# Kernel optimization log

Hardware: AMD Instinct MI355X
Metric: run time of the kernel (lower is better)

Reference implementation:

```python
import jax, jax.numpy as jnp
import numpy as np

B, T, S, O, D = 1024, 512, 8, 4, 64  # batch, seq_len, sensory_dim, output_dim, hidden d (d=64 from target_params=78980)


def _w(key, shape):
    # random weights scaled ~1/sqrt(fan_in); stored as [in, out] so y = x @ W + b
    return jax.random.normal(key, shape, dtype=jnp.float32) / np.sqrt(shape[0]).astype(np.float32)


def setup_inputs() -> dict:
    key = jax.random.key(0)
    ks = jax.random.split(key, 16)
    z = lambda n: jnp.zeros((n,), jnp.float32)
    return {
        "x": jax.random.normal(ks[0], (B, T, S), dtype=jnp.float32),
        "W_enc_w": _w(ks[1], (S, D)), "W_enc_b": z(D),
        "W_from_W": _w(ks[2], (D, D)), "W_from_I": _w(ks[3], (D, D)), "W_from_A": _w(ks[4], (D, D)),
        "W_gate_w": _w(ks[5], (2 * D, D)), "W_gate_b": z(D),
        "I_z_w": _w(ks[6], (3 * D, D)), "I_z_b": z(D),
        "I_r_w": _w(ks[7], (3 * D, D)), "I_r_b": z(D),
        "I_h_w": _w(ks[8], (3 * D, D)), "I_h_b": z(D),
        "A_from_W": _w(ks[9], (D, D)), "A_from_I": _w(ks[10], (D, D)), "A_from_A": _w(ks[11], (D, D)),
        "A_gate_w": _w(ks[12], (2 * D, D)), "A_gate_b": z(D),
        "phi_w": _w(ks[13], (D, O)), "phi_b": z(O),
    }


def reference(x, W_enc_w, W_enc_b, W_from_W, W_from_I, W_from_A, W_gate_w, W_gate_b,
              I_z_w, I_z_b, I_r_w, I_r_b, I_h_w, I_h_b,
              A_from_W, A_from_I, A_from_A, A_gate_w, A_gate_b, phi_w, phi_b):
    batch = x.shape[0]
    d = W_from_W.shape[0]

    def step(carry, x_t):
        W, I, A = carry  # each [B, d]
        xt = jnp.tanh(x_t @ W_enc_w + W_enc_b)
        W_in = xt + W @ W_from_W + I @ W_from_I + A @ W_from_A
        Wg = jax.nn.sigmoid(jnp.concatenate([I, A], -1) @ W_gate_w + W_gate_b)
        W_new = jnp.tanh(W_in) * Wg
        comb = jnp.concatenate([W_new, I, A], -1)  # [B, 3d]
        z = jax.nn.sigmoid(comb @ I_z_w + I_z_b)
        r = jax.nn.sigmoid(comb @ I_r_w + I_r_b)
        h = jnp.tanh(jnp.concatenate([W_new, r * I, A], -1) @ I_h_w + I_h_b)
        I_new = (1.0 - z) * I + z * h
        A_in = W_new @ A_from_W + I_new @ A_from_I + A @ A_from_A
        Ag = jax.nn.sigmoid(jnp.concatenate([W_new, I_new], -1) @ A_gate_w + A_gate_b)
        A_new = jnp.tanh(A_in) * Ag
        action = A_new @ phi_w + phi_b  # [B, O]
        return (W_new, I_new, A_new), action

    init = tuple(jnp.zeros((batch, d), x.dtype) for _ in range(3))
    _, actions = jax.lax.scan(step, init, jnp.swapaxes(x, 0, 1))  # [T, B, O]
    return jnp.swapaxes(actions, 0, 1)  # [B, T, O]
```

## Files before the change

### kernel.cpp

```cpp
#include <hip/hip_runtime.h>
#include <cstddef>
#include <cstdint>

#define T_LEN 512
#define O_DIM 4

typedef _Float16 f16x8 __attribute__((ext_vector_type(8)));
typedef float    f32x4 __attribute__((ext_vector_type(4)));

#define MFMA(a, b, c) __builtin_amdgcn_mfma_f32_16x16x32_f16((a), (b), (c), 0, 0, 0)

__device__ __forceinline__ float sigm_f(float x) {
    return __builtin_amdgcn_rcpf(1.0f + __builtin_amdgcn_exp2f(x * -1.44269504f));
}
__device__ __forceinline__ float tanh_f(float x) {
    float e = __builtin_amdgcn_exp2f(x * 2.88539008f);
    return __builtin_fmaf(-2.0f, __builtin_amdgcn_rcpf(e + 1.0f), 1.0f);
}

__device__ __forceinline__ f16x8 load_bt(const float* __restrict__ W, int k0, int n) {
    const int lane = threadIdx.x & 63;
    const float* p = W + (size_t)(k0 + ((lane >> 4) << 3)) * 64 + n;
    f16x8 r;
#pragma unroll
    for (int j = 0; j < 8; ++j) r[j] = (_Float16)p[(size_t)j * 64];
    return r;
}

__device__ __forceinline__ f16x8 ld_af(const _Float16* base, int kt) {
    const int lane = threadIdx.x & 63;
    const int m = lane & 15, q = lane >> 4;
    return *(const f16x8*)(base + m * 72 + kt * 32 + q * 8);
}

__global__ __launch_bounds__(256, 1) void ANIMAZeroExact_86887188398421_kernel(
    const float* __restrict__ x,
    const float* __restrict__ Wenc_w, const float* __restrict__ Wenc_b,
    const float* __restrict__ WfW, const float* __restrict__ WfI, const float* __restrict__ WfA,
    const float* __restrict__ Wg_w, const float* __restrict__ Wg_b,
    const float* __restrict__ Iz_w, const float* __restrict__ Iz_b,
    const float* __restrict__ Ir_w, const float* __restrict__ Ir_b,
    const float* __restrict__ Ih_w, const float* __restrict__ Ih_b,
    const float* __restrict__ AfW, const float* __restrict__ AfI, const float* __restrict__ AfA,
    const float* __restrict__ Ag_w, const float* __restrict__ Ag_b,
    const float* __restrict__ phi_w, const float* __restrict__ phi_b,
    float* __restrict__ out)
{
    __shared__ __align__(16) _Float16 Wl[16][72];
    __shared__ __align__(16) _Float16 Il[16][72];
    __shared__ __align__(16) _Float16 Al[16][72];
    __shared__ __align__(16) _Float16 Rl[16][72];
    __shared__ __align__(16) float actb[4][16][4];

    const int tid  = threadIdx.x;
    const int w    = tid >> 6;
    const int lane = tid & 63;
    const int q    = lane >> 4;
    const int c    = lane & 15;
    const int n    = w * 16 + c;
    const int r0   = blockIdx.x * 4;

    for (int i = tid; i < 16 * 72; i += 256) {
        (&Wl[0][0])[i] = (_Float16)0.0f; (&Il[0][0])[i] = (_Float16)0.0f;
        (&Al[0][0])[i] = (_Float16)0.0f; (&Rl[0][0])[i] = (_Float16)0.0f;
    }

    f16x8 S1B[6], G1B[4], ZB[6], RB[6], HB[6], AB[6], AGB[4], phiB[2];
#pragma unroll
    for (int j = 0; j < 2; ++j) {
        S1B[j] = load_bt(WfW, 32 * j, n);  S1B[2 + j] = load_bt(WfI, 32 * j, n);  S1B[4 + j] = load_bt(WfA, 32 * j, n);
        AB[j]  = load_bt(AfW, 32 * j, n);  AB[2 + j]  = load_bt(AfI, 32 * j, n);  AB[4 + j]  = load_bt(AfA, 32 * j, n);
    }
#pragma unroll
    for (int j = 0; j < 4; ++j) { G1B[j] = load_bt(Wg_w, 32 * j, n); AGB[j] = load_bt(Ag_w, 32 * j, n); }
#pragma unroll
    for (int j = 0; j < 6; ++j) { ZB[j] = load_bt(Iz_w, 32 * j, n); RB[j] = load_bt(Ir_w, 32 * j, n); HB[j] = load_bt(Ih_w, 32 * j, n); }
#pragma unroll
    for (int kt = 0; kt < 2; ++kt)
#pragma unroll
        for (int j = 0; j < 8; ++j) {
            int k = kt * 32 + q * 8 + j;
            phiB[kt][j] = (c < O_DIM && w == 0) ? (_Float16)phi_w[k * O_DIM + c] : (_Float16)0.0f;
        }

    float We[8];
#pragma unroll
    for (int j = 0; j < 8; ++j) We[j] = Wenc_w[j * 64 + n];

    const float bias_g  = Wg_b[n],  bias_z = Iz_b[n], bias_r = Ir_b[n];
    const float bias_h  = Ih_b[n],  bias_ag = Ag_b[n], bias_e = Wenc_b[n];
    const float bias_p  = (c < O_DIM) ? phi_b[c] : 0.0f;

    const float* xrow = x + (size_t)(r0 + q) * (T_LEN * 8);

    f32x4 zero4 = {0.f, 0.f, 0.f, 0.f};

    float xt;
    {
        float4 a = *(const float4*)(xrow);
        float4 b = *(const float4*)(xrow + 4);
        float d = bias_e;
        d = __builtin_fmaf(a.x, We[0], d); d = __builtin_fmaf(a.y, We[1], d);
        d = __builtin_fmaf(a.z, We[2], d); d = __builtin_fmaf(a.w, We[3], d);
        d = __builtin_fmaf(b.x, We[4], d); d = __builtin_fmaf(b.y, We[5], d);
        d = __builtin_fmaf(b.z, We[6], d); d = __builtin_fmaf(b.w, We[7], d);
        xt = tanh_f(d);
    }

    f32x4 w_a = zero4, w_b = zero4, g_a = zero4, g_b = zero4;
    f32x4 zp_a = zero4, zp_c = zero4, rp_a = zero4, rp_c = zero4;
    f32x4 hp_a, hp_c, ap_a, ap_c, ag_a, ag_c;
    float Iv = 0.f;
    f16x8 nW0, nW1;

    __syncthreads();

#pragma unroll 1
    for (int t = 0; t < T_LEN; ++t) {
        const bool fl = ((t & 15) == 0) && (t > 0);

        int tn = (t + 1 < T_LEN) ? t + 1 : t;
        float4 xa = *(const float4*)(xrow + (size_t)tn * 8);
        float4 xb = *(const float4*)(xrow + (size_t)tn * 8 + 4);

        f16x8 sA0 = ld_af(&Al[0][0], 0), sA1 = ld_af(&Al[0][0], 1);
        w_a = MFMA(sA0, S1B[4], w_a);  w_b = MFMA(sA1, S1B[5], w_b);
        g_a = MFMA(sA0, G1B[2], g_a);  g_b = MFMA(sA1, G1B[3], g_b);
        {
            float wn = tanh_f(xt + w_a[0] + w_b[0]) * sigm_f(g_a[0] + g_b[0] + bias_g);
            Wl[4 * q][n] = (_Float16)wn;
        }
        zp_a = MFMA(sA0, ZB[4], zp_a);  zp_c = MFMA(sA1, ZB[5], zp_c);
        rp_a = MFMA(sA0, RB[4], rp_a);  rp_c = MFMA(sA1, RB[5], rp_c);
        hp_a = MFMA(sA0, HB[4], zero4); hp_c = MFMA(sA1, HB[5], zero4);
        ap_a = MFMA(sA0, AB[4], zero4); ap_c = MFMA(sA1, AB[5], zero4);
        if (w == 0) {
            f32x4 act = MFMA(sA0, phiB[0], zero4);
            act = MFMA(sA1, phiB[1], act);
            if (t > 0 && c < O_DIM)
                actb[q][(t - 1) & 15][c] = act[0] + bias_p;
        }
        __syncthreads();

        nW0 = ld_af(&Wl[0][0], 0); nW1 = ld_af(&Wl[0][0], 1);
        rp_a = MFMA(nW0, RB[0], rp_a);  rp_c = MFMA(nW1, RB[1], rp_c);
        {
            float rv = sigm_f(rp_a[0] + rp_c[0] + bias_r);
            Rl[4 * q][n] = (_Float16)(rv * Iv);
        }
        zp_a = MFMA(nW0, ZB[0], zp_a);  zp_c = MFMA(nW1, ZB[1], zp_c);
        float zv = sigm_f(zp_a[0] + zp_c[0] + bias_z);
        hp_a = MFMA(nW0, HB[0], hp_a);  hp_c = MFMA(nW1, HB[1], hp_c);
        ap_a = MFMA(nW0, AB[0], ap_a);  ap_c = MFMA(nW1, AB[1], ap_c);
        ag_a = MFMA(nW0, AGB[0], zero4); ag_c = MFMA(nW1, AGB[1], zero4);
        if (fl && tid < 64) {
            int row = tid >> 4, sl = tid & 15;
            float4 av = *(const float4*)(&actb[row][sl][0]);
            *(float4*)(out + (size_t)(r0 + row) * (T_LEN * O_DIM) + (t - 16 + sl) * 4) = av;
        }
        __syncthreads();

        f16x8 hR0 = ld_af(&Rl[0][0], 0), hR1 = ld_af(&Rl[0][0], 1);
        hp_a = MFMA(hR0, HB[2], hp_a);  hp_c = MFMA(hR1, HB[3], hp_c);
        {
            float hv = tanh_f(hp_a[0] + hp_c[0] + bias_h);
            Iv = __builtin_fmaf(zv, hv - Iv, Iv);
            Il[4 * q][n] = (_Float16)Iv;
        }
        {
            float d = bias_e;
            d = __builtin_fmaf(xa.x, We[0], d); d = __builtin_fmaf(xa.y, We[1], d);
            d = __builtin_fmaf(xa.z, We[2], d); d = __builtin_fmaf(xa.w, We[3], d);
            d = __builtin_fmaf(xb.x, We[4], d); d = __builtin_fmaf(xb.y, We[5], d);
            d = __builtin_fmaf(xb.z, We[6], d); d = __builtin_fmaf(xb.w, We[7], d);
            xt = tanh_f(d);
        }
        __syncthreads();

        f16x8 nI0 = ld_af(&Il[0][0], 0), nI1 = ld_af(&Il[0][0], 1);
        ap_a = MFMA(nI0, AB[2], ap_a);  ap_c = MFMA(nI1, AB[3], ap_c);
        ag_a = MFMA(nI0, AGB[2], ag_a); ag_c = MFMA(nI1, AGB[3], ag_c);
        {
            float av = tanh_f(ap_a[0] + ap_c[0]) * sigm_f(ag_a[0] + ag_c[0] + bias_ag);
            Al[4 * q][n] = (_Float16)av;
        }
        w_a = MFMA(nW0, S1B[0], zero4);  w_b = MFMA(nW1, S1B[1], zero4);
        w_a = MFMA(nI0, S1B[2], w_a);    w_b = MFMA(nI1, S1B[3], w_b);
        g_a = MFMA(nI0, G1B[0], zero4);  g_b = MFMA(nI1, G1B[1], zero4);
        zp_a = MFMA(nI0, ZB[2], zero4);  zp_c = MFMA(nI1, ZB[3], zero4);
        rp_a = MFMA(nI0, RB[2], zero4);  rp_c = MFMA(nI1, RB[3], zero4);
        __syncthreads();
    }

    {
        f16x8 eA0 = ld_af(&Al[0][0], 0), eA1 = ld_af(&Al[0][0], 1);
        if (w == 0) {
            f32x4 act = MFMA(eA0, phiB[0], zero4);
            act = MFMA(eA1, phiB[1], act);
            if (c < O_DIM)
                actb[q][15][c] = act[0] + bias_p;
        }
        __syncthreads();
        if (tid < 64) {
            int row = tid >> 4, sl = tid & 15;
            float4 av = *(const float4*)(&actb[row][sl][0]);
            *(float4*)(out + (size_t)(r0 + row) * (T_LEN * O_DIM) + (496 + sl) * 4) = av;
        }
    }
}

extern "C" void kernel_launch(void* const* d_in, const int* in_sizes, int n_in,
                              void* d_out, int out_size, void* d_ws, size_t ws_size,
                              hipStream_t stream) {
    ANIMAZeroExact_86887188398421_kernel<<<dim3(256), dim3(256), 0, stream>>>(
        (const float*)d_in[0],
        (const float*)d_in[1],  (const float*)d_in[2],
        (const float*)d_in[3],  (const float*)d_in[4],  (const float*)d_in[5],
        (const float*)d_in[6],  (const float*)d_in[7],
        (const float*)d_in[8],  (const float*)d_in[9],
        (const float*)d_in[10], (const float*)d_in[11],
        (const float*)d_in[12], (const float*)d_in[13],
        (const float*)d_in[14], (const float*)d_in[15], (const float*)d_in[16],
        (const float*)d_in[17], (const float*)d_in[18],
        (const float*)d_in[19], (const float*)d_in[20],
        (float*)d_out);
}
```

Before: 562.9 us.

## Stage x inputs through LDS tiles and reschedule MFMAs across barriers

Replaces the per-step global load of the next x row with a shared-memory tile that 64 threads refill every 16 steps. The refill's global loads are issued early and stored to LDS later in the step. The MFMA schedule is also reordered: the Z/R MFMAs on the I state move to the start of the next iteration, and the S1B W-term MFMA moves earlier, spreading matrix work more evenly between the four barriers. The aim is to take global-load latency off the serial recurrence and shorten the critical path per step. The cost is extra LDS traffic and more complex timing of when the tile is refilled.

```diff
diff --git a/kernel.cpp b/kernel.cpp
--- a/kernel.cpp
+++ b/kernel.cpp
@@ -16,6 +16,13 @@
 __device__ __forceinline__ float tanh_f(float x) {
     float e = __builtin_amdgcn_exp2f(x * 2.88539008f);
     return __builtin_fmaf(-2.0f, __builtin_amdgcn_rcpf(e + 1.0f), 1.0f);
+}
+
+__device__ __forceinline__ f16x8 zf8() {
+    f16x8 r;
+#pragma unroll
+    for (int j = 0; j < 8; ++j) r[j] = (_Float16)0.0f;
+    return r;
 }
 
 __device__ __forceinline__ f16x8 load_bt(const float* __restrict__ W, int k0, int n) {
@@ -50,6 +57,7 @@
     __shared__ __align__(16) _Float16 Il[16][72];
     __shared__ __align__(16) _Float16 Al[16][72];
     __shared__ __align__(16) _Float16 Rl[16][72];
+    __shared__ __align__(16) float xtile[4 * 132 + 4];
     __shared__ __align__(16) float actb[4][16][4];
 
     const int tid  = threadIdx.x;
@@ -91,14 +99,21 @@
     const float bias_h  = Ih_b[n],  bias_ag = Ag_b[n], bias_e = Wenc_b[n];
     const float bias_p  = (c < O_DIM) ? phi_b[c] : 0.0f;
 
-    const float* xrow = x + (size_t)(r0 + q) * (T_LEN * 8);
-
     f32x4 zero4 = {0.f, 0.f, 0.f, 0.f};
 
+    if (tid < 64) {
+        const int row = tid >> 4, su = tid & 15;
+        const float* xg = x + (size_t)(r0 + row) * (T_LEN * 8) + (1 + su) * 8;
+        float4 a = *(const float4*)(xg);
+        float4 b = *(const float4*)(xg + 4);
+        float* d = &xtile[row * 132 + su * 8];
+        *(float4*)d = a; *(float4*)(d + 4) = b;
+    }
     float xt;
     {
-        float4 a = *(const float4*)(xrow);
-        float4 b = *(const float4*)(xrow + 4);
+        const float* xg = x + (size_t)(r0 + q) * (T_LEN * 8);
+        float4 a = *(const float4*)(xg);
+        float4 b = *(const float4*)(xg + 4);
         float d = bias_e;
         d = __builtin_fmaf(a.x, We[0], d); d = __builtin_fmaf(a.y, We[1], d);
         d = __builtin_fmaf(a.z, We[2], d); d = __builtin_fmaf(a.w, We[3], d);
@@ -107,11 +122,10 @@
         xt = tanh_f(d);
     }
 
+    f16x8 nI0 = zf8(), nI1 = zf8(), nW0, nW1;
     f32x4 w_a = zero4, w_b = zero4, g_a = zero4, g_b = zero4;
-    f32x4 zp_a = zero4, zp_c = zero4, rp_a = zero4, rp_c = zero4;
-    f32x4 hp_a, hp_c, ap_a, ap_c, ag_a, ag_c;
+    f32x4 zp_a, zp_c, rp_a, rp_c, hp_a, hp_c, ap_a, ap_c, ag_a, ag_c;
     float Iv = 0.f;
-    f16x8 nW0, nW1;
 
     __syncthreads();
 
@@ -119,76 +133,88 @@
     for (int t = 0; t < T_LEN; ++t) {
         const bool fl = ((t & 15) == 0) && (t > 0);
 
-        int tn = (t + 1 < T_LEN) ? t + 1 : t;
-        float4 xa = *(const float4*)(xrow + (size_t)tn * 8);
-        float4 xb = *(const float4*)(xrow + (size_t)tn * 8 + 4);
-
         f16x8 sA0 = ld_af(&Al[0][0], 0), sA1 = ld_af(&Al[0][0], 1);
+        float4 xla = {0,0,0,0}, xlb = {0,0,0,0};
+        if (fl && tid < 64) {
+            const int row = tid >> 4, su = tid & 15;
+            int off = (t + 1 + su) * 8;
+            if (off > T_LEN * 8 - 8) off = T_LEN * 8 - 8;
+            const float* xg = x + (size_t)(r0 + row) * (T_LEN * 8) + off;
+            xla = *(const float4*)(xg); xlb = *(const float4*)(xg + 4);
+        }
+        zp_a = MFMA(nI0, ZB[2], zero4); zp_c = MFMA(nI1, ZB[3], zero4);
+        rp_a = MFMA(nI0, RB[2], zero4); rp_c = MFMA(nI1, RB[3], zero4);
         w_a = MFMA(sA0, S1B[4], w_a);  w_b = MFMA(sA1, S1B[5], w_b);
         g_a = MFMA(sA0, G1B[2], g_a);  g_b = MFMA(sA1, G1B[3], g_b);
         {
             float wn = tanh_f(xt + w_a[0] + w_b[0]) * sigm_f(g_a[0] + g_b[0] + bias_g);
             Wl[4 * q][n] = (_Float16)wn;
         }
+        __syncthreads();
+
+        nW0 = ld_af(&Wl[0][0], 0); nW1 = ld_af(&Wl[0][0], 1);
+        hp_a = MFMA(sA0, HB[4], zero4); hp_c = MFMA(sA1, HB[5], zero4);
+        ap_a = MFMA(sA0, AB[4], zero4); ap_c = MFMA(sA1, AB[5], zero4);
         zp_a = MFMA(sA0, ZB[4], zp_a);  zp_c = MFMA(sA1, ZB[5], zp_c);
         rp_a = MFMA(sA0, RB[4], rp_a);  rp_c = MFMA(sA1, RB[5], rp_c);
-        hp_a = MFMA(sA0, HB[4], zero4); hp_c = MFMA(sA1, HB[5], zero4);
-        ap_a = MFMA(sA0, AB[4], zero4); ap_c = MFMA(sA1, AB[5], zero4);
         if (w == 0) {
             f32x4 act = MFMA(sA0, phiB[0], zero4);
             act = MFMA(sA1, phiB[1], act);
             if (t > 0 && c < O_DIM)
                 actb[q][(t - 1) & 15][c] = act[0] + bias_p;
         }
-        __syncthreads();
-
-        nW0 = ld_af(&Wl[0][0], 0); nW1 = ld_af(&Wl[0][0], 1);
         rp_a = MFMA(nW0, RB[0], rp_a);  rp_c = MFMA(nW1, RB[1], rp_c);
         {
             float rv = sigm_f(rp_a[0] + rp_c[0] + bias_r);
             Rl[4 * q][n] = (_Float16)(rv * Iv);
         }
         zp_a = MFMA(nW0, ZB[0], zp_a);  zp_c = MFMA(nW1, ZB[1], zp_c);
-        float zv = sigm_f(zp_a[0] + zp_c[0] + bias_z);
+        if (fl && tid < 64) {
+            const int row = tid >> 4, su = tid & 15;
+            float* d = &xtile[row * 132 + su * 8];
+            *(float4*)d = xla; *(float4*)(d + 4) = xlb;
+        }
+        __syncthreads();
+
+        f16x8 hR0 = ld_af(&Rl[0][0], 0), hR1 = ld_af(&Rl[0][0], 1);
+        const float* xs = &xtile[q * 132 + (t & 15) * 8];
+        float4 qa = *(const float4*)xs;
+        float4 qb = *(const float4*)(xs + 4);
         hp_a = MFMA(nW0, HB[0], hp_a);  hp_c = MFMA(nW1, HB[1], hp_c);
         ap_a = MFMA(nW0, AB[0], ap_a);  ap_c = MFMA(nW1, AB[1], ap_c);
         ag_a = MFMA(nW0, AGB[0], zero4); ag_c = MFMA(nW1, AGB[1], zero4);
+        w_a  = MFMA(nW0, S1B[0], zero4); w_b = MFMA(nW1, S1B[1], zero4);
+        float zv = sigm_f(zp_a[0] + zp_c[0] + bias_z);
         if (fl && tid < 64) {
-            int row = tid >> 4, sl = tid & 15;
+            const int row = tid >> 4, sl = tid & 15;
             float4 av = *(const float4*)(&actb[row][sl][0]);
             *(float4*)(out + (size_t)(r0 + row) * (T_LEN * O_DIM) + (t - 16 + sl) * 4) = av;
         }
-        __syncthreads();
-
-        f16x8 hR0 = ld_af(&Rl[0][0], 0), hR1 = ld_af(&Rl[0][0], 1);
         hp_a = MFMA(hR0, HB[2], hp_a);  hp_c = MFMA(hR1, HB[3], hp_c);
         {
             float hv = tanh_f(hp_a[0] + hp_c[0] + bias_h);
             Iv = __builtin_fmaf(zv, hv - Iv, Iv);
             Il[4 * q][n] = (_Float16)Iv;
         }
+        __syncthreads();
+
+        nI0 = ld_af(&Il[0][0], 0); nI1 = ld_af(&Il[0][0], 1);
         {
             float d = bias_e;
-            d = __builtin_fmaf(xa.x, We[0], d); d = __builtin_fmaf(xa.y, We[1], d);
-            d = __builtin_fmaf(xa.z, We[2], d); d = __builtin_fmaf(xa.w, We[3], d);
-            d = __builtin_fmaf(xb.x, We[4], d); d = __builtin_fmaf(xb.y, We[5], d);
-            d = __builtin_fmaf(xb.z, We[6], d); d = __builtin_fmaf(xb.w, We[7], d);
+            d = __builtin_fmaf(qa.x, We[0], d); d = __builtin_fmaf(qa.y, We[1], d);
+            d = __builtin_fmaf(qa.z, We[2], d); d = __builtin_fmaf(qa.w, We[3], d);
+            d = __builtin_fmaf(qb.x, We[4], d); d = __builtin_fmaf(qb.y, We[5], d);
+            d = __builtin_fmaf(qb.z, We[6], d); d = __builtin_fmaf(qb.w, We[7], d);
             xt = tanh_f(d);
         }
-        __syncthreads();
-
-        f16x8 nI0 = ld_af(&Il[0][0], 0), nI1 = ld_af(&Il[0][0], 1);
         ap_a = MFMA(nI0, AB[2], ap_a);  ap_c = MFMA(nI1, AB[3], ap_c);
         ag_a = MFMA(nI0, AGB[2], ag_a); ag_c = MFMA(nI1, AGB[3], ag_c);
         {
             float av = tanh_f(ap_a[0] + ap_c[0]) * sigm_f(ag_a[0] + ag_c[0] + bias_ag);
             Al[4 * q][n] = (_Float16)av;
         }
-        w_a = MFMA(nW0, S1B[0], zero4);  w_b = MFMA(nW1, S1B[1], zero4);
-        w_a = MFMA(nI0, S1B[2], w_a);    w_b = MFMA(nI1, S1B[3], w_b);
-        g_a = MFMA(nI0, G1B[0], zero4);  g_b = MFMA(nI1, G1B[1], zero4);
-        zp_a = MFMA(nI0, ZB[2], zero4);  zp_c = MFMA(nI1, ZB[3], zero4);
-        rp_a = MFMA(nI0, RB[2], zero4);  rp_c = MFMA(nI1, RB[3], zero4);
+        w_a = MFMA(nI0, S1B[2], w_a);   w_b = MFMA(nI1, S1B[3], w_b);
+        g_a = MFMA(nI0, G1B[0], zero4); g_b = MFMA(nI1, G1B[1], zero4);
         __syncthreads();
     }
 
@@ -202,7 +228,7 @@
         }
         __syncthreads();
         if (tid < 64) {
-            int row = tid >> 4, sl = tid & 15;
+            const int row = tid >> 4, sl = tid & 15;
             float4 av = *(const float4*)(&actb[row][sl][0]);
             *(float4*)(out + (size_t)(r0 + row) * (T_LEN * O_DIM) + (496 + sl) * 4) = av;
         }
```

New measurement: 518.0 us. 8.0% less time.
